# Optimization experiments

Measured on AMD Instinct MI355X. Metric: run time of the kernel, lower is better.

Reference implementation:

```python
import jax, jax.numpy as jnp
import numpy as np

B, C, D, H, W = 8, 1, 160, 160, 160
SPATIAL_AXES = (2, 3, 4)  # axial, coronal, sagittal map to dims D, H, W


def setup_inputs() -> dict:
    key = jax.random.key(0)
    k1, _ = jax.random.split(key)
    x = jax.random.normal(k1, (B, C, D, H, W), dtype=jnp.float32)
    log_sigma = jnp.zeros((3,), dtype=jnp.float32)  # log(initial_sigma=1.0)
    return {"x": x, "log_sigma": log_sigma}


def reference(x, log_sigma):
    # For each spatial axis: adjacent-slice diff, squared distance summed over
    # channel + remaining spatial dims (per batch, per slice-pair), RBF kernel,
    # then -mean over (batch, slice-pairs). Equivalent to the original
    # sum_i(-mean_b(k_i)) / (n_slices - 1) since mean is linear.
    sigma = jnp.exp(log_sigma)
    total = jnp.float32(0.0)
    for i, ax in enumerate(SPATIAL_AXES):
        d = jnp.diff(x, axis=ax)  # [B, C, ...] with S-1 along ax
        reduce_dims = tuple(a for a in range(5) if a not in (0, ax))
        sq = jnp.sum(d * d, axis=reduce_dims)  # [B, S-1]
        k = jnp.exp(-sq / (2.0 * sigma[i] ** 2))
        total = total + (-jnp.mean(k))
    return total / jnp.float32(len(SPATIAL_AXES))
```

## Files before the change

### kernel.cpp

```cpp
#include <hip/hip_runtime.h>


constexpr int Wd4 = 40;
constexpr int SLICE4 = 6400;
constexpr long BSTR4 = 160L * 6400;
constexpr int NB = 8;
constexpr int NPAIR = 159;
constexpr int NKEY = 3 * NB * NPAIR;
constexpr int SLOT = 200;
constexpr int NBLK = NB * 160;
constexpr int PART_OFF = NBLK * SLOT;
constexpr int NFIN = 60;

__device__ __forceinline__ float sq4(const float4& a, const float4& c) {
    float e0 = a.x - c.x, e1 = a.y - c.y, e2 = a.z - c.z, e3 = a.w - c.w;
    return e0 * e0 + e1 * e1 + e2 * e2 + e3 * e3;
}

__global__ __launch_bounds__(320) void diff3_kernel(const float* __restrict__ x,
                                                    float* __restrict__ ws) {
    __shared__ float lds[1504];

    const int t = threadIdx.x;
    const int bid = blockIdx.x;
    const int b = bid / 160;
    const int r2 = bid % 160;
    const int ds = r2 / 5;
    const int hc = r2 % 5;
    const int d0 = ds * 5, h0 = hc * 32;
    const bool lastSeg = (ds == 31);

    const int c4 = t % 40;
    const int rp = t / 40;
    const int lane = t & 63;
    const int wv = t >> 6;
    const bool hOK = !(hc == 4 && rp == 7);
    const bool sOK = (c4 < 39);
    const bool fixB = (lane == 63) && sOK;

    const float4* base = (const float4*)x + (size_t)b * BSTR4 + (size_t)d0 * SLICE4
                       + (size_t)(h0 + 4 * rp) * Wd4 + c4;

    float aW[4] = {0.f, 0.f, 0.f, 0.f};
    float aH[4] = {0.f, 0.f, 0.f, 0.f};
    float aD[5] = {0.f, 0.f, 0.f, 0.f, 0.f};
    float4 p0, p1, p2, p3;

#pragma unroll
    for (int it = 0; it < 5; ++it) {
        const float4* sp = base + it * SLICE4;
        const float4 v0 = sp[0];
        const float4 v1 = sp[Wd4];
        const float4 v2 = sp[2 * Wd4];
        const float4 v3 = sp[3 * Wd4];
        float4 hv;
        if (hOK) hv = sp[4 * Wd4];
        float bx0 = 0.f, bx1 = 0.f, bx2 = 0.f, bx3 = 0.f;
        if (fixB) {
            bx0 = ((const float*)(sp))[4];
            bx1 = ((const float*)(sp + Wd4))[4];
            bx2 = ((const float*)(sp + 2 * Wd4))[4];
            bx3 = ((const float*)(sp + 3 * Wd4))[4];
        }
        float s0 = __shfl_down(v0.x, 1, 64); if (fixB) s0 = bx0;
        float s1 = __shfl_down(v1.x, 1, 64); if (fixB) s1 = bx1;
        float s2 = __shfl_down(v2.x, 1, 64); if (fixB) s2 = bx2;
        float s3 = __shfl_down(v3.x, 1, 64); if (fixB) s3 = bx3;

        float dw;
        dw = v0.y - v0.x; aW[0] += dw * dw;
        dw = v0.z - v0.y; aW[1] += dw * dw;
        dw = v0.w - v0.z; aW[2] += dw * dw;
        dw = v1.y - v1.x; aW[0] += dw * dw;
        dw = v1.z - v1.y; aW[1] += dw * dw;
        dw = v1.w - v1.z; aW[2] += dw * dw;
        dw = v2.y - v2.x; aW[0] += dw * dw;
        dw = v2.z - v2.y; aW[1] += dw * dw;
        dw = v2.w - v2.z; aW[2] += dw * dw;
        dw = v3.y - v3.x; aW[0] += dw * dw;
        dw = v3.z - v3.y; aW[1] += dw * dw;
        dw = v3.w - v3.z; aW[2] += dw * dw;
        if (sOK) {
            dw = s0 - v0.w; aW[3] += dw * dw;
            dw = s1 - v1.w; aW[3] += dw * dw;
            dw = s2 - v2.w; aW[3] += dw * dw;
            dw = s3 - v3.w; aW[3] += dw * dw;
        }
        aH[0] += sq4(v1, v0);
        aH[1] += sq4(v2, v1);
        aH[2] += sq4(v3, v2);
        if (hOK) aH[3] += sq4(hv, v3);
        if (it > 0)
            aD[it - 1] += sq4(v0, p0) + sq4(v1, p1) + sq4(v2, p2) + sq4(v3, p3);
        p0 = v0; p1 = v1; p2 = v2; p3 = v3;
    }
    if (!lastSeg) {
        const float4* sp = base + 5 * SLICE4;
        aD[4] = sq4(sp[0], p0) + sq4(sp[Wd4], p1) + sq4(sp[2 * Wd4], p2) + sq4(sp[3 * Wd4], p3);
    }

#pragma unroll
    for (int j = 0; j < 4; ++j) lds[(4 * rp + j) * 41 + c4] = aH[j];
#pragma unroll
    for (int j = 0; j < 5; ++j) {
        float dd = aD[j];
        for (int off = 32; off > 0; off >>= 1) dd += __shfl_down(dd, off, 64);
        if (lane == 0) lds[1472 + j * 5 + wv] = dd;
    }
    __syncthreads();
    float hsum = 0.f, dsum = 0.f;
    if (t < 32) {
        const float* src = &lds[t * 41];
        for (int i = 0; i < 40; ++i) hsum += src[i];
    }
    if (t < 5) {
        for (int w2 = 0; w2 < 5; ++w2) dsum += lds[1472 + t * 5 + w2];
    }
    __syncthreads();
#pragma unroll
    for (int j = 0; j < 4; ++j) lds[(4 * c4 + j) * 9 + rp] = aW[j];
    __syncthreads();
    float wsum = 0.f;
    if (t < 160) {
        const float* src = &lds[t * 9];
        for (int i = 0; i < 8; ++i) wsum += src[i];
    }
    float* slot = ws + (size_t)bid * SLOT;
    if (t < 5)   slot[t] = dsum;
    if (t < 32)  slot[5 + t] = hsum;
    if (t < 160) slot[37 + t] = wsum;
}

__global__ __launch_bounds__(64) void reduce_kernel(const float* __restrict__ ws,
                                                    const float* __restrict__ log_sigma,
                                                    float* __restrict__ part) {
    const int gk = blockIdx.x * 64 + threadIdx.x;
    float kv = 0.f;
    if (gk < NKEY) {
        const int a = gk / (NB * NPAIR);
        const int rem = gk % (NB * NPAIR);
        const int b = rem / NPAIR;
        const int k = rem % NPAIR;
        const float f = -0.5f * expf(-2.f * log_sigma[a]);
        const float* bb = ws + (size_t)b * 160 * SLOT;
        float val = 0.f;
        if (a == 0) {
            const int ds = k / 5, j = k % 5;
            const float* p = bb + (size_t)(ds * 5) * SLOT + j;
            for (int hc = 0; hc < 5; ++hc) val += p[hc * SLOT];
        } else if (a == 1) {
            const int hc = k / 32, kk = k % 32;
            const float* p = bb + (size_t)hc * SLOT + 5 + kk;
            for (int ds = 0; ds < 32; ++ds) val += p[(size_t)(ds * 5) * SLOT];
        } else {
            const float* p = bb + 37 + k;
            for (int i = 0; i < 160; ++i) val += p[(size_t)i * SLOT];
        }
        kv = expf(val * f);
    }
    for (int off = 32; off > 0; off >>= 1) kv += __shfl_down(kv, off, 64);
    if (threadIdx.x == 0) part[blockIdx.x] = kv;
}

__global__ __launch_bounds__(64) void final_kernel(const float* __restrict__ part,
                                                   float* __restrict__ out) {
    float v = (threadIdx.x < NFIN) ? part[threadIdx.x] : 0.f;
    for (int off = 32; off > 0; off >>= 1) v += __shfl_down(v, off, 64);
    if (threadIdx.x == 0) out[0] = -v / (float)NKEY;
}

extern "C" void kernel_launch(void* const* d_in, const int* in_sizes, int n_in,
                              void* d_out, int out_size, void* d_ws, size_t ws_size,
                              hipStream_t stream) {
    const float* x = (const float*)d_in[0];
    const float* log_sigma = (const float*)d_in[1];
    float* out = (float*)d_out;
    float* ws = (float*)d_ws;

    diff3_kernel<<<NBLK, 320, 0, stream>>>(x, ws);
    reduce_kernel<<<NFIN, 64, 0, stream>>>(ws, log_sigma, ws + PART_OFF);
    final_kernel<<<1, 64, 0, stream>>>(ws + PART_OFF, out);
}
```

Measured before the change: 196.5 us.

## Transpose partial-sum workspace layout and fold final reduction into atomics

The first kernel now writes its per-block partial sums in a key-major transposed layout, so the reduce kernel reads them with coalesced accesses instead of strided per-block slots. The separate final kernel is dropped: each reduce block atomically adds its scaled partial into the output, which the first kernel zeroes. This removes one launch and the uncoalesced reads in exchange for float atomic ordering nondeterminism.

```diff
diff --git a/kernel.cpp b/kernel.cpp
--- a/kernel.cpp
+++ b/kernel.cpp
@@ -6,11 +6,12 @@
 constexpr long BSTR4 = 160L * 6400;
 constexpr int NB = 8;
 constexpr int NPAIR = 159;
-constexpr int NKEY = 3 * NB * NPAIR;
-constexpr int SLOT = 200;
+constexpr int PBATCH = NB * NPAIR;
+constexpr int NKEY = 3 * PBATCH;
 constexpr int NBLK = NB * 160;
-constexpr int PART_OFF = NBLK * SLOT;
-constexpr int NFIN = 60;
+constexpr int NRED = 60;
+constexpr int HT_OFF = 5 * PBATCH;
+constexpr int WT_OFF = 37 * PBATCH;
 
 __device__ __forceinline__ float sq4(const float4& a, const float4& c) {
     float e0 = a.x - c.x, e1 = a.y - c.y, e2 = a.z - c.z, e3 = a.w - c.w;
@@ -18,7 +19,8 @@
 }
 
 __global__ __launch_bounds__(320) void diff3_kernel(const float* __restrict__ x,
-                                                    float* __restrict__ ws) {
+                                                    float* __restrict__ ws,
+                                                    float* __restrict__ out) {
     __shared__ float lds[1504];
 
     const int t = threadIdx.x;
@@ -37,6 +39,8 @@
     const bool hOK = !(hc == 4 && rp == 7);
     const bool sOK = (c4 < 39);
     const bool fixB = (lane == 63) && sOK;
+
+    if (bid == 0 && t == 0) out[0] = 0.f;
 
     const float4* base = (const float4*)x + (size_t)b * BSTR4 + (size_t)d0 * SLICE4
                        + (size_t)(h0 + 4 * rp) * Wd4 + c4;
@@ -125,48 +129,34 @@
         const float* src = &lds[t * 9];
         for (int i = 0; i < 8; ++i) wsum += src[i];
     }
-    float* slot = ws + (size_t)bid * SLOT;
-    if (t < 5)   slot[t] = dsum;
-    if (t < 32)  slot[5 + t] = hsum;
-    if (t < 160) slot[37 + t] = wsum;
+
+    const int kb = b * NPAIR;
+    if (t < 5 && (d0 + t) < NPAIR)  ws[hc * PBATCH + kb + d0 + t] = dsum;
+    if (t < 32 && (h0 + t) < NPAIR) ws[HT_OFF + ds * PBATCH + kb + h0 + t] = hsum;
+    if (t < NPAIR)                  ws[WT_OFF + r2 * PBATCH + kb + t] = wsum;
 }
 
 __global__ __launch_bounds__(64) void reduce_kernel(const float* __restrict__ ws,
                                                     const float* __restrict__ log_sigma,
-                                                    float* __restrict__ part) {
+                                                    float* __restrict__ out) {
     const int gk = blockIdx.x * 64 + threadIdx.x;
     float kv = 0.f;
     if (gk < NKEY) {
-        const int a = gk / (NB * NPAIR);
-        const int rem = gk % (NB * NPAIR);
-        const int b = rem / NPAIR;
-        const int k = rem % NPAIR;
+        const int a = gk / PBATCH;
+        const int rem = gk % PBATCH;
         const float f = -0.5f * expf(-2.f * log_sigma[a]);
-        const float* bb = ws + (size_t)b * 160 * SLOT;
         float val = 0.f;
         if (a == 0) {
-            const int ds = k / 5, j = k % 5;
-            const float* p = bb + (size_t)(ds * 5) * SLOT + j;
-            for (int hc = 0; hc < 5; ++hc) val += p[hc * SLOT];
+            for (int hc = 0; hc < 5; ++hc)   val += ws[hc * PBATCH + rem];
         } else if (a == 1) {
-            const int hc = k / 32, kk = k % 32;
-            const float* p = bb + (size_t)hc * SLOT + 5 + kk;
-            for (int ds = 0; ds < 32; ++ds) val += p[(size_t)(ds * 5) * SLOT];
+            for (int dss = 0; dss < 32; ++dss) val += ws[HT_OFF + dss * PBATCH + rem];
         } else {
-            const float* p = bb + 37 + k;
-            for (int i = 0; i < 160; ++i) val += p[(size_t)i * SLOT];
+            for (int ci = 0; ci < 160; ++ci) val += ws[WT_OFF + ci * PBATCH + rem];
         }
         kv = expf(val * f);
     }
     for (int off = 32; off > 0; off >>= 1) kv += __shfl_down(kv, off, 64);
-    if (threadIdx.x == 0) part[blockIdx.x] = kv;
-}
-
-__global__ __launch_bounds__(64) void final_kernel(const float* __restrict__ part,
-                                                   float* __restrict__ out) {
-    float v = (threadIdx.x < NFIN) ? part[threadIdx.x] : 0.f;
-    for (int off = 32; off > 0; off >>= 1) v += __shfl_down(v, off, 64);
-    if (threadIdx.x == 0) out[0] = -v / (float)NKEY;
+    if (threadIdx.x == 0) atomicAdd(out, -kv / (float)NKEY);
 }
 
 extern "C" void kernel_launch(void* const* d_in, const int* in_sizes, int n_in,
@@ -177,7 +167,6 @@
     float* out = (float*)d_out;
     float* ws = (float*)d_ws;
 
-    diff3_kernel<<<NBLK, 320, 0, stream>>>(x, ws);
-    reduce_kernel<<<NFIN, 64, 0, stream>>>(ws, log_sigma, ws + PART_OFF);
-    final_kernel<<<1, 64, 0, stream>>>(ws + PART_OFF, out);
+    diff3_kernel<<<NBLK, 320, 0, stream>>>(x, ws, out);
+    reduce_kernel<<<NRED, 64, 0, stream>>>(ws, log_sigma, out);
 }
```

New measurement: 197.0 us. No clear change (+0.2%).
